# Optimization experiments

Measured on AMD Instinct MI355X. Metric: run time of the kernel, lower is better.

Reference implementation:

```python
import jax, jax.numpy as jnp
import numpy as np

B, T, H = 2048, 512, 16  # batch, seq_len, lstm hidden


def _lstm_step(h, c, x_t, W_ih, W_hh, b):
    # PyTorch gate order: i, f, g, o ; z: [B, 4H]
    z = x_t @ W_ih.T + h @ W_hh.T + b
    i, f, g, o = jnp.split(z, 4, axis=-1)
    c = jax.nn.sigmoid(f) * c + jax.nn.sigmoid(i) * jnp.tanh(g)
    h = jax.nn.sigmoid(o) * jnp.tanh(c)
    return h, c


def setup_inputs() -> dict:
    key = jax.random.key(0)
    ks = jax.random.split(key, 14)
    s = 1.0 / np.sqrt(H)  # torch default uniform init bound
    u = lambda k, shp: jax.random.uniform(k, shp, jnp.float32, -s, s)
    return {
        "x": jax.random.normal(ks[0], (B, T, 1), jnp.float32),
        # forward-direction LSTM params
        "W_ih_f": u(ks[1], (4 * H, 1)),
        "W_hh_f": u(ks[2], (4 * H, H)),
        "b_ih_f": u(ks[3], (4 * H,)),
        "b_hh_f": u(ks[4], (4 * H,)),
        # reverse-direction LSTM params
        "W_ih_r": u(ks[5], (4 * H, 1)),
        "W_hh_r": u(ks[6], (4 * H, H)),
        "b_ih_r": u(ks[7], (4 * H,)),
        "b_hh_r": u(ks[8], (4 * H,)),
        # MLP head (Dropout is identity at inference)
        "W1": u(ks[9], (16, 32)),
        "b1": u(ks[10], (16,)),
        "W2": u(ks[11], (1, 16)),
        "b2": u(ks[12], (1,)),
    }


def reference(x, W_ih_f, W_hh_f, b_ih_f, b_hh_f,
              W_ih_r, W_hh_r, b_ih_r, b_hh_r, W1, b1, W2, b2):
    Bv = x.shape[0]
    h0 = jnp.zeros((Bv, H), x.dtype)
    b_f = b_ih_f + b_hh_f

    # forward direction: out[:, -1, :H] is the final forward hidden state
    def step(carry, x_t):
        h, c = carry
        h, c = _lstm_step(h, c, x_t, W_ih_f, W_hh_f, b_f)
        return (h, c), None

    (h_fwd, _), _ = jax.lax.scan(step, (h0, h0), jnp.swapaxes(x, 0, 1))

    # reverse direction at t = T-1 is the FIRST step of the reverse scan,
    # i.e. one LSTM step on x[:, -1] from zero state (only part sliced by out[:, -1]).
    h_bwd, _ = _lstm_step(h0, h0, x[:, -1], W_ih_r, W_hh_r, b_ih_r + b_hh_r)

    h_cat = jnp.concatenate([h_fwd, h_bwd], axis=-1)  # [B, 32]
    # Dropout(0.5) is identity in eval mode
    hid = h_cat @ W1.T + b1
    hid = jnp.where(hid > 0, hid, 0.2 * hid)  # LeakyReLU(0.2)
    return hid @ W2.T + b2  # [B, 1]
```

## Files before the change

kernel.cpp:

```cpp
#include <hip/hip_runtime.h>

#define T_LEN 512
#define LOG2E 1.4426950408889634f

typedef float f32x2 __attribute__((ext_vector_type(2)));

__device__ __forceinline__ float rl(float v, int lane) {
    return __int_as_float(__builtin_amdgcn_readlane(__float_as_int(v), lane));
}
template<int CTRL>
__device__ __forceinline__ float qperm(float v) {
    return __int_as_float(__builtin_amdgcn_mov_dpp(__float_as_int(v), CTRL, 0xF, 0xF, true));
}

__global__ __launch_bounds__(256, 2) void bilstm_head_kernel(
    const float* __restrict__ x,
    const float* __restrict__ W_ih_f, const float* __restrict__ W_hh_f,
    const float* __restrict__ b_ih_f, const float* __restrict__ b_hh_f,
    const float* __restrict__ W_ih_r, const float* __restrict__ W_hh_r,
    const float* __restrict__ b_ih_r, const float* __restrict__ b_hh_r,
    const float* __restrict__ W1, const float* __restrict__ b1,
    const float* __restrict__ W2, const float* __restrict__ b2,
    float* __restrict__ out)
{
    extern __shared__ float smem[];

    const int tid  = threadIdx.x;
    const int wid  = tid >> 6;
    const int lane = tid & 63;
    const int b    = blockIdx.x * 4 + wid;

    const int gate = lane & 3;
    const int k    = lane >> 2;
    const int row  = gate * 16 + k;

    const bool  isg = (gate == 2);
    const float c1  = isg ? (-2.0f * LOG2E) : (-LOG2E);
    const float cm  = isg ? 2.0f : 1.0f;
    const float ca  = isg ? -1.0f : 0.0f;
    const float k2  = -2.0f * LOG2E;

    const float wih_p  = W_ih_f[row] * c1;
    const float bias_p = (b_ih_f[row] + b_hh_f[row]) * c1;
    f32x2 wp[8];
#pragma unroll
    for (int n = 0; n < 8; ++n) {
        wp[n].x = W_hh_f[row * 16 + 2 * n]     * c1;
        wp[n].y = W_hh_f[row * 16 + 2 * n + 1] * c1;
    }

    const int wfl = wid * 592;
#pragma unroll
    for (int i = 0; i < 8; ++i)
        smem[wfl + 64 + i * 64 + lane] = x[b * T_LEN + i * 64 + lane];

    const unsigned hbase = (unsigned)(wfl * 4);
    unsigned xaddr = hbase + 224;
    const unsigned waddr = hbase + (unsigned)(row * 4);
    float c = 0.0f;

    if ((blockIdx.x >> 8) & 1) __builtin_amdgcn_s_sleep(2);

#define LSTM_STEP(XC, XN, XOFF) \
    "s_waitcnt lgkmcnt(5)\n\t" \
    "v_fma_f32 v20, " XC ", %[wih], %[bias]\n\t" \
    "v_mov_b32 v21, 0\n\t" \
    "s_waitcnt lgkmcnt(3)\n\t" \
    "v_pk_fma_f32 v[20:21], v[32:33], %[w01], v[20:21]\n\t" \
    "v_pk_fma_f32 v[20:21], v[34:35], %[w23], v[20:21]\n\t" \
    "s_waitcnt lgkmcnt(2)\n\t" \
    "v_pk_fma_f32 v[20:21], v[36:37], %[w45], v[20:21]\n\t" \
    "v_pk_fma_f32 v[20:21], v[38:39], %[w67], v[20:21]\n\t" \
    "s_waitcnt lgkmcnt(1)\n\t" \
    "v_pk_mul_f32 v[24:25], v[40:41], %[w89]\n\t" \
    "v_pk_fma_f32 v[24:25], v[42:43], %[wAB], v[24:25]\n\t" \
    "s_waitcnt lgkmcnt(0)\n\t" \
    "v_pk_fma_f32 v[24:25], v[44:45], %[wCD], v[24:25]\n\t" \
    "v_pk_fma_f32 v[24:25], v[46:47], %[wEF], v[24:25]\n\t" \
    "v_pk_add_f32 v[20:21], v[20:21], v[24:25]\n\t" \
    "v_add_f32 v20, v20, v21\n\t" \
    "v_exp_f32 v22, v20\n\t" \
    "ds_read_b32 " XN ", %[vX] offset:" XOFF "\n\t" \
    "s_nop 0\n\t" \
    "v_add_f32 v22, 1.0, v22\n\t" \
    "v_rcp_f32 v22, v22\n\t" \
    "s_nop 1\n\t" \
    "v_fma_f32 v23, v22, %[cm], %[ca]\n\t" \
    "s_nop 1\n\t" \
    "v_mov_b32_dpp v26, v23 quad_perm:[1,0,3,2] row_mask:0xf bank_mask:0xf\n\t" \
    "v_mul_f32_dpp v22, v23, v23 quad_perm:[2,3,0,1] row_mask:0xf bank_mask:0xf\n\t" \
    "s_nop 0\n\t" \
    "v_fma_f32 %[c], v26, %[c], v22\n\t" \
    "v_mul_f32 v22, %[k2], %[c]\n\t" \
    "v_exp_f32 v22, v22\n\t" \
    "s_nop 1\n\t" \
    "v_add_f32 v22, 1.0, v22\n\t" \
    "v_rcp_f32 v22, v22\n\t" \
    "s_nop 1\n\t" \
    "v_fma_f32 v22, v22, 2.0, -1.0\n\t" \
    "v_mul_f32_dpp v29, v23, v22 quad_perm:[3,2,1,0] row_mask:0xf bank_mask:0xf\n\t" \
    "s_nop 0\n\t" \
    "ds_write_b32 %[vW], v29\n\t" \
    "ds_read_b128 v[32:35], %[vB] offset:0\n\t" \
    "ds_read_b128 v[36:39], %[vB] offset:16\n\t" \
    "ds_read_b128 v[40:43], %[vB] offset:32\n\t" \
    "ds_read_b128 v[44:47], %[vB] offset:48\n\t"

    asm volatile(
        "v_mov_b32 v29, 0\n\t"
        "ds_read_b32 v30, %[vB] offset:256\n\t"
        "ds_write_b32 %[vW], v29\n\t"
        "ds_read_b128 v[32:35], %[vB] offset:0\n\t"
        "ds_read_b128 v[36:39], %[vB] offset:16\n\t"
        "ds_read_b128 v[40:43], %[vB] offset:32\n\t"
        "ds_read_b128 v[44:47], %[vB] offset:48\n\t"
        "s_mov_b32 s20, 0\n\t"
        "1:\n\t"
        "v_add_u32 %[vX], 32, %[vX]\n\t"
        LSTM_STEP("v30", "v31", "4")
        LSTM_STEP("v31", "v30", "8")
        LSTM_STEP("v30", "v31", "12")
        LSTM_STEP("v31", "v30", "16")
        LSTM_STEP("v30", "v31", "20")
        LSTM_STEP("v31", "v30", "24")
        LSTM_STEP("v30", "v31", "28")
        LSTM_STEP("v31", "v30", "32")
        "s_add_u32 s20, s20, 1\n\t"
        "s_cmp_lt_u32 s20, 64\n\t"
        "s_cbranch_scc1 1b\n\t"
        "s_waitcnt lgkmcnt(0)\n\t"
        : [c]"+v"(c), [vX]"+v"(xaddr)
        : [vB]"v"(hbase), [vW]"v"(waddr),
          [wih]"v"(wih_p), [bias]"v"(bias_p),
          [cm]"v"(cm), [ca]"v"(ca), [k2]"v"(k2),
          [w01]"v"(wp[0]), [w23]"v"(wp[1]), [w45]"v"(wp[2]), [w67]"v"(wp[3]),
          [w89]"v"(wp[4]), [wAB]"v"(wp[5]), [wCD]"v"(wp[6]), [wEF]"v"(wp[7])
        : "v20","v21","v22","v23","v24","v25","v26","v27","v28","v29",
          "v30","v31","v32","v33","v34","v35","v36","v37","v38","v39",
          "v40","v41","v42","v43","v44","v45","v46","v47",
          "s20","scc","memory");
#undef LSTM_STEP

    float hs[16];
#pragma unroll
    for (int n = 0; n < 16; ++n) hs[n] = smem[wfl + n];

    const float wihr  = W_ih_r[row];
    const float biasr = b_ih_r[row] + b_hh_r[row];
    const float xlast = smem[wfl + 64 + 511];

    const float zr   = fmaf(xlast, wihr, biasr);
    const float er   = __builtin_amdgcn_exp2f(zr * c1);
    const float rr_  = __builtin_amdgcn_rcpf(1.0f + er);
    const float actr = fmaf(rr_, cm, ca);
    const float gr   = qperm<0x4E>(actr);
    const float or_  = qperm<0x1B>(actr);
    const float cr   = actr * gr;
    const float e2r  = __builtin_amdgcn_exp2f(cr * (-2.0f * LOG2E));
    const float thr_ = fmaf(__builtin_amdgcn_rcpf(1.0f + e2r), 2.0f, -1.0f);
    const float hbw  = or_ * thr_;

    float hr[16];
#pragma unroll
    for (int n = 0; n < 16; ++n) hr[n] = rl(hbw, 4 * n);

    const int m = lane & 15;
    float hid = b1[m];
#pragma unroll
    for (int n = 0; n < 16; ++n) hid = fmaf(hs[n], W1[m * 32 + n], hid);
#pragma unroll
    for (int n = 0; n < 16; ++n) hid = fmaf(hr[n], W1[m * 32 + 16 + n], hid);
    hid = (hid > 0.0f) ? hid : (0.2f * hid);

    float v = hid * W2[m];
    v += __shfl_xor(v, 1);
    v += __shfl_xor(v, 2);
    v += __shfl_xor(v, 4);
    v += __shfl_xor(v, 8);
    if (lane == 0) out[b] = v + b2[0];
}

extern "C" void kernel_launch(void* const* d_in, const int* in_sizes, int n_in,
                              void* d_out, int out_size, void* d_ws, size_t ws_size,
                              hipStream_t stream) {
    const float* x      = (const float*)d_in[0];
    const float* W_ih_f = (const float*)d_in[1];
    const float* W_hh_f = (const float*)d_in[2];
    const float* b_ih_f = (const float*)d_in[3];
    const float* b_hh_f = (const float*)d_in[4];
    const float* W_ih_r = (const float*)d_in[5];
    const float* W_hh_r = (const float*)d_in[6];
    const float* b_ih_r = (const float*)d_in[7];
    const float* b_hh_r = (const float*)d_in[8];
    const float* W1     = (const float*)d_in[9];
    const float* b1     = (const float*)d_in[10];
    const float* W2     = (const float*)d_in[11];
    const float* b2     = (const float*)d_in[12];
    float* out = (float*)d_out;

    const int B = in_sizes[0] / T_LEN;
    dim3 grid(B / 4), block(256);
    size_t lds_bytes = 4 * 592 * sizeof(float);
    hipLaunchKernelGGL(bilstm_head_kernel, grid, block, lds_bytes, stream,
                       x, W_ih_f, W_hh_f, b_ih_f, b_hh_f,
                       W_ih_r, W_hh_r, b_ih_r, b_hh_r,
                       W1, b1, W2, b2, out);
}
```

Baseline: 76.92 us.

## Batch x prefetch as b128 reads, rebalance FMA chains, use 512-thread blocks

Result: faster. 75.27 us (-2.1%).

```diff
diff --git a/kernel.cpp b/kernel.cpp
--- a/kernel.cpp
+++ b/kernel.cpp
@@ -13,7 +13,7 @@
     return __int_as_float(__builtin_amdgcn_mov_dpp(__float_as_int(v), CTRL, 0xF, 0xF, true));
 }
 
-__global__ __launch_bounds__(256, 2) void bilstm_head_kernel(
+__global__ __launch_bounds__(512, 1) void bilstm_head_kernel(
     const float* __restrict__ x,
     const float* __restrict__ W_ih_f, const float* __restrict__ W_hh_f,
     const float* __restrict__ b_ih_f, const float* __restrict__ b_hh_f,
@@ -28,7 +28,7 @@
     const int tid  = threadIdx.x;
     const int wid  = tid >> 6;
     const int lane = tid & 63;
-    const int b    = blockIdx.x * 4 + wid;
+    const int b    = blockIdx.x * 8 + wid;
 
     const int gate = lane & 3;
     const int k    = lane >> 2;
@@ -54,33 +54,32 @@
     for (int i = 0; i < 8; ++i)
         smem[wfl + 64 + i * 64 + lane] = x[b * T_LEN + i * 64 + lane];
 
-    const unsigned hbase = (unsigned)(wfl * 4);
-    unsigned xaddr = hbase + 224;
-    const unsigned waddr = hbase + (unsigned)(row * 4);
+    const unsigned vB = (unsigned)(wfl * 4);
+    const unsigned vW = vB + (unsigned)(row * 4);
+    unsigned vX = (unsigned)((wfl + 64) * 4);
     float c = 0.0f;
 
-    if ((blockIdx.x >> 8) & 1) __builtin_amdgcn_s_sleep(2);
-
-#define LSTM_STEP(XC, XN, XOFF) \
-    "s_waitcnt lgkmcnt(5)\n\t" \
+    if (wid & 4) __builtin_amdgcn_s_sleep(2);
+
+#define LSTM_STEP(XC, FILL) \
     "v_fma_f32 v20, " XC ", %[wih], %[bias]\n\t" \
     "v_mov_b32 v21, 0\n\t" \
     "s_waitcnt lgkmcnt(3)\n\t" \
     "v_pk_fma_f32 v[20:21], v[32:33], %[w01], v[20:21]\n\t" \
     "v_pk_fma_f32 v[20:21], v[34:35], %[w23], v[20:21]\n\t" \
     "s_waitcnt lgkmcnt(2)\n\t" \
-    "v_pk_fma_f32 v[20:21], v[36:37], %[w45], v[20:21]\n\t" \
-    "v_pk_fma_f32 v[20:21], v[38:39], %[w67], v[20:21]\n\t" \
+    "v_pk_mul_f32 v[24:25], v[36:37], %[w45]\n\t" \
+    "v_pk_fma_f32 v[24:25], v[38:39], %[w67], v[24:25]\n\t" \
     "s_waitcnt lgkmcnt(1)\n\t" \
-    "v_pk_mul_f32 v[24:25], v[40:41], %[w89]\n\t" \
+    "v_pk_fma_f32 v[20:21], v[40:41], %[w89], v[20:21]\n\t" \
     "v_pk_fma_f32 v[24:25], v[42:43], %[wAB], v[24:25]\n\t" \
     "s_waitcnt lgkmcnt(0)\n\t" \
-    "v_pk_fma_f32 v[24:25], v[44:45], %[wCD], v[24:25]\n\t" \
+    "v_pk_fma_f32 v[20:21], v[44:45], %[wCD], v[20:21]\n\t" \
     "v_pk_fma_f32 v[24:25], v[46:47], %[wEF], v[24:25]\n\t" \
     "v_pk_add_f32 v[20:21], v[20:21], v[24:25]\n\t" \
     "v_add_f32 v20, v20, v21\n\t" \
     "v_exp_f32 v22, v20\n\t" \
-    "ds_read_b32 " XN ", %[vX] offset:" XOFF "\n\t" \
+    FILL \
     "s_nop 0\n\t" \
     "v_add_f32 v22, 1.0, v22\n\t" \
     "v_rcp_f32 v22, v22\n\t" \
@@ -106,40 +105,51 @@
     "ds_read_b128 v[40:43], %[vB] offset:32\n\t" \
     "ds_read_b128 v[44:47], %[vB] offset:48\n\t"
 
+#define NOFILL "s_nop 0\n\t"
+#define FILLA  "ds_read_b128 v[8:11], %[vX] offset:32\n\t"
+#define FILLB  "ds_read_b128 v[12:15], %[vX] offset:48\n\t"
+
     asm volatile(
+        "s_waitcnt lgkmcnt(0)\n\t"
         "v_mov_b32 v29, 0\n\t"
-        "ds_read_b32 v30, %[vB] offset:256\n\t"
+        "ds_read_b128 v[8:11],  %[vX] offset:0\n\t"
+        "ds_read_b128 v[12:15], %[vX] offset:16\n\t"
         "ds_write_b32 %[vW], v29\n\t"
         "ds_read_b128 v[32:35], %[vB] offset:0\n\t"
         "ds_read_b128 v[36:39], %[vB] offset:16\n\t"
         "ds_read_b128 v[40:43], %[vB] offset:32\n\t"
         "ds_read_b128 v[44:47], %[vB] offset:48\n\t"
+        "s_waitcnt lgkmcnt(4)\n\t"
         "s_mov_b32 s20, 0\n\t"
         "1:\n\t"
+        LSTM_STEP("v8",  NOFILL)
+        LSTM_STEP("v9",  NOFILL)
+        LSTM_STEP("v10", NOFILL)
+        LSTM_STEP("v11", FILLA)
+        LSTM_STEP("v12", NOFILL)
+        LSTM_STEP("v13", NOFILL)
+        LSTM_STEP("v14", NOFILL)
+        LSTM_STEP("v15", FILLB)
         "v_add_u32 %[vX], 32, %[vX]\n\t"
-        LSTM_STEP("v30", "v31", "4")
-        LSTM_STEP("v31", "v30", "8")
-        LSTM_STEP("v30", "v31", "12")
-        LSTM_STEP("v31", "v30", "16")
-        LSTM_STEP("v30", "v31", "20")
-        LSTM_STEP("v31", "v30", "24")
-        LSTM_STEP("v30", "v31", "28")
-        LSTM_STEP("v31", "v30", "32")
         "s_add_u32 s20, s20, 1\n\t"
         "s_cmp_lt_u32 s20, 64\n\t"
         "s_cbranch_scc1 1b\n\t"
         "s_waitcnt lgkmcnt(0)\n\t"
-        : [c]"+v"(c), [vX]"+v"(xaddr)
-        : [vB]"v"(hbase), [vW]"v"(waddr),
+        : [c]"+v"(c), [vX]"+v"(vX)
+        : [vB]"v"(vB), [vW]"v"(vW),
           [wih]"v"(wih_p), [bias]"v"(bias_p),
           [cm]"v"(cm), [ca]"v"(ca), [k2]"v"(k2),
           [w01]"v"(wp[0]), [w23]"v"(wp[1]), [w45]"v"(wp[2]), [w67]"v"(wp[3]),
           [w89]"v"(wp[4]), [wAB]"v"(wp[5]), [wCD]"v"(wp[6]), [wEF]"v"(wp[7])
-        : "v20","v21","v22","v23","v24","v25","v26","v27","v28","v29",
-          "v30","v31","v32","v33","v34","v35","v36","v37","v38","v39",
+        : "v8","v9","v10","v11","v12","v13","v14","v15",
+          "v20","v21","v22","v23","v24","v25","v26","v27","v28","v29",
+          "v32","v33","v34","v35","v36","v37","v38","v39",
           "v40","v41","v42","v43","v44","v45","v46","v47",
           "s20","scc","memory");
 #undef LSTM_STEP
+#undef NOFILL
+#undef FILLA
+#undef FILLB
 
     float hs[16];
 #pragma unroll
@@ -199,8 +209,8 @@
     float* out = (float*)d_out;
 
     const int B = in_sizes[0] / T_LEN;
-    dim3 grid(B / 4), block(256);
-    size_t lds_bytes = 4 * 592 * sizeof(float);
+    dim3 grid(B / 8), block(512);
+    size_t lds_bytes = 8 * 592 * sizeof(float);
     hipLaunchKernelGGL(bilstm_head_kernel, grid, block, lds_bytes, stream,
                        x, W_ih_f, W_hh_f, b_ih_f, b_hh_f,
                        W_ih_r, W_hh_r, b_ih_r, b_hh_r,
```
